# Kernel optimization log

Hardware: AMD Instinct MI355X
Metric: run time of the kernel (lower is better)

Reference implementation:

```python
import jax, jax.numpy as jnp
import numpy as np

B, S, D = 4, 2048, 1024
H, E = 8, 128  # num_head, num_dim (per-head)

def setup_inputs() -> dict:
    key = jax.random.key(0)
    ks = jax.random.split(key, 8)
    scale_in = 1.0 / np.sqrt(D)
    return {
        "q": jax.random.normal(ks[0], (B, S, D), dtype=jnp.float32),
        "k": jax.random.normal(ks[1], (B, S, D), dtype=jnp.float32),
        "v": jax.random.normal(ks[2], (B, S, D), dtype=jnp.float32),
        "Wq": jax.random.normal(ks[3], (H, D, E), dtype=jnp.float32) * scale_in,
        "Wk": jax.random.normal(ks[4], (H, D, E), dtype=jnp.float32) * scale_in,
        "Wv": jax.random.normal(ks[5], (H, D, E), dtype=jnp.float32) * scale_in,
        "Wo": jax.random.normal(ks[6], (H * E, D), dtype=jnp.float32) * (1.0 / np.sqrt(H * E)),
        "bo": jnp.zeros((D,), dtype=jnp.float32),
    }

def reference(q, k, v, Wq, Wk, Wv, Wo, bo):
    dk = jnp.asarray(E, q.dtype) ** 0.5
    # per-head projections, all heads batched: [B,H,S,E]
    qh = jnp.einsum("bsd,hde->bhse", q, Wq)
    kh = jnp.einsum("bsd,hde->bhse", k, Wk)
    vh = jnp.einsum("bsd,hde->bhse", v, Wv)
    scores = jnp.einsum("bhse,bhte->bhst", qh / dk, kh)  # [B,H,S,S]
    attn = jax.nn.softmax(scores, axis=-1)
    zh = jnp.einsum("bhst,bhte->bhse", attn, vh)  # [B,H,S,E]
    # concat heads along feature dim (head order preserved): [B,S,H*E]
    z = jnp.transpose(zh, (0, 2, 1, 3)).reshape(B, S, H * E)
    return z @ Wo + bo
```

## Files before the change

kernel.cpp:

```cpp
#include <hip/hip_runtime.h>

#define B_ 4
#define S_ 2048
#define D_ 1024
#define H_ 8
#define E_ 128

typedef __bf16 bf16_t;
typedef __bf16 bf16x8 __attribute__((ext_vector_type(8)));
typedef float f32x4 __attribute__((ext_vector_type(4)));

#define MFMA16(a, b, c) __builtin_amdgcn_mfma_f32_16x16x32_bf16(a, b, c, 0, 0, 0)

#define LDP_ 72

__device__ __forceinline__ void load_lds16(const bf16_t* g, bf16_t* l) {
    __builtin_amdgcn_global_load_lds(
        (const __attribute__((address_space(1))) unsigned int*)g,
        (__attribute__((address_space(3))) unsigned int*)l,
        16, 0, 0);
}

__device__ __forceinline__ f32x4 zero4() {
    f32x4 z = {0.f, 0.f, 0.f, 0.f};
    return z;
}

__global__ __launch_bounds__(64) void detect_dtype(const unsigned int* __restrict__ q,
                                                   int* __restrict__ flag) {
    int lane = threadIdx.x;
    int cnt = 0;
    for (int i = lane; i < 4096; i += 64) {
        unsigned e = (q[i] >> 7) & 0xFFu;
        cnt += (e >= 110u && e <= 141u) ? 1 : 0;
    }
#pragma unroll
    for (int d = 32; d; d >>= 1) cnt += __shfl_down(cnt, d);
    if (lane == 0) *flag = (cnt > 2048) ? 1 : 0;
}

__global__ __launch_bounds__(256) void convert_bf16(const void* __restrict__ in,
                                                    bf16_t* __restrict__ out,
                                                    const int* __restrict__ flagp) {
    int isb = *flagp;
    size_t i = ((size_t)blockIdx.x * 256 + threadIdx.x) * 8;
    if (isb) {
        *(bf16x8*)(out + i) = *(const bf16x8*)((const bf16_t*)in + i);
    } else {
        const float* p = (const float*)in + i;
        f32x4 lo = *(const f32x4*)p;
        f32x4 hi = *(const f32x4*)(p + 4);
        bf16x8 v;
#pragma unroll
        for (int j = 0; j < 4; j++) { v[j] = (bf16_t)lo[j]; v[4 + j] = (bf16_t)hi[j]; }
        *(bf16x8*)(out + i) = v;
    }
}

__global__ __launch_bounds__(256) void transpose_any(const void* __restrict__ in,
                                                     bf16_t* __restrict__ out,
                                                     int R, int C,
                                                     const int* __restrict__ flagp) {
    __shared__ bf16_t tile[32][33];
    int isb = *flagp;
    int bz = blockIdx.z;
    const bf16_t* inb16 = (const bf16_t*)in + (size_t)bz * R * C;
    const float*  inb32 = (const float*)in + (size_t)bz * R * C;
    bf16_t* outb = out + (size_t)bz * R * C;
    int tx = threadIdx.x & 31, ty = threadIdx.x >> 5;
    int r0 = blockIdx.y * 32, c0 = blockIdx.x * 32;
#pragma unroll
    for (int i = 0; i < 4; i++) {
        size_t idx = (size_t)(r0 + ty + i * 8) * C + c0 + tx;
        tile[ty + i * 8][tx] = isb ? inb16[idx] : (bf16_t)inb32[idx];
    }
    __syncthreads();
#pragma unroll
    for (int i = 0; i < 4; i++)
        outb[(size_t)(c0 + ty + i * 8) * R + r0 + tx] = tile[tx][ty + i * 8];
}

__global__ __launch_bounds__(256) void proj_gemm(const bf16_t* __restrict__ A,
                                                 const bf16_t* __restrict__ Wt,
                                                 bf16_t* __restrict__ Out,
                                                 int vmode, float oscale) {
    __shared__ __align__(16) bf16_t Alds[128 * 32];
    __shared__ __align__(16) bf16_t Blds[128 * 32];
    int m0 = blockIdx.x * 128;
    int h = blockIdx.y;
    const bf16_t* Bt = Wt + (size_t)h * E_ * D_;
    int t = threadIdx.x;
    int w = t >> 6, lane = t & 63;
    int quad = lane >> 4, ln = lane & 15;
    int wm = (w >> 1) * 64, wn = (w & 1) * 64;

    f32x4 acc[4][4];
#pragma unroll
    for (int i = 0; i < 4; i++)
#pragma unroll
        for (int j = 0; j < 4; j++) acc[i][j] = zero4();

    for (int k0 = 0; k0 < D_; k0 += 32) {
#pragma unroll
        for (int i = 0; i < 2; i++) {
            int base = i * 256 + w * 64;
            int G = base + lane;
            int r = G >> 2, c = (G & 3) ^ (r & 3);
            load_lds16(A + (size_t)(m0 + r) * D_ + k0 + c * 8, Alds + (size_t)base * 8);
            load_lds16(Bt + (size_t)r * D_ + k0 + c * 8, Blds + (size_t)base * 8);
        }
        asm volatile("s_waitcnt vmcnt(0)" ::: "memory");
        __syncthreads();

        bf16x8 af[4], bfr[4];
#pragma unroll
        for (int mt = 0; mt < 4; mt++) {
            int row = wm + mt * 16 + ln;
            af[mt] = *(const bf16x8*)(Alds + (size_t)row * 32 + (quad ^ (ln & 3)) * 8);
        }
#pragma unroll
        for (int nt = 0; nt < 4; nt++) {
            int row = wn + nt * 16 + ln;
            bfr[nt] = *(const bf16x8*)(Blds + (size_t)row * 32 + (quad ^ (ln & 3)) * 8);
        }
#pragma unroll
        for (int mt = 0; mt < 4; mt++)
#pragma unroll
            for (int nt = 0; nt < 4; nt++)
                acc[mt][nt] = MFMA16(af[mt], bfr[nt], acc[mt][nt]);
        __syncthreads();
    }

#pragma unroll
    for (int mt = 0; mt < 4; mt++) {
#pragma unroll
        for (int nt = 0; nt < 4; nt++) {
#pragma unroll
            for (int r = 0; r < 4; r++) {
                int grow = m0 + wm + mt * 16 + quad * 4 + r;
                int e = wn + nt * 16 + ln;
                int b = grow >> 11;
                int s = grow & 2047;
                float v = acc[mt][nt][r] * oscale;
                size_t idx;
                if (vmode == 0)
                    idx = ((size_t)((b * H_ + h) * S_ + s)) * E_ + e;
                else
                    idx = ((size_t)((b * H_ + h) * E_ + e)) * S_ + s;
                Out[idx] = (bf16_t)v;
            }
        }
    }
}

__global__ __launch_bounds__(256, 3) void flash_attn(const bf16_t* __restrict__ Qh,
                                                     const bf16_t* __restrict__ Kh,
                                                     const bf16_t* __restrict__ Vt,
                                                     bf16_t* __restrict__ Z) {
    __shared__ __align__(16) bf16_t Klds[64 * 128];
    __shared__ __align__(16) bf16_t Vlds[128 * 64];
    __shared__ __align__(16) bf16_t Plds[4 * 32 * LDP_];
    int bh = blockIdx.y;
    int qt = blockIdx.x;
    const bf16_t* Qbh = Qh + (size_t)bh * S_ * E_;
    const bf16_t* Kbh = Kh + (size_t)bh * S_ * E_;
    const bf16_t* Vbh = Vt + (size_t)bh * E_ * S_;
    int t = threadIdx.x, w = t >> 6, lane = t & 63;
    int quad = lane >> 4, ln = lane & 15;
    bf16_t* Pw = Plds + w * 32 * LDP_;

    bf16x8 qf[2][4];
#pragma unroll
    for (int mt = 0; mt < 2; mt++)
#pragma unroll
        for (int ks = 0; ks < 4; ks++)
            qf[mt][ks] = *(const bf16x8*)(Qbh + (size_t)(qt * 128 + w * 32 + mt * 16 + ln) * E_ +
                                          ks * 32 + quad * 8);

    f32x4 oacc[2][8];
#pragma unroll
    for (int mt = 0; mt < 2; mt++)
#pragma unroll
        for (int nt = 0; nt < 8; nt++) oacc[mt][nt] = zero4();
    float rsum[2][4];
#pragma unroll
    for (int mt = 0; mt < 2; mt++)
#pragma unroll
        for (int r = 0; r < 4; r++) rsum[mt][r] = 0.f;

    for (int kt = 0; kt < S_ / 64; kt++) {
#pragma unroll
        for (int j = 0; j < 4; j++) {
            int base = j * 256 + w * 64;
            int G = base + lane;
            int rK = G >> 4, cK = (G & 15) ^ (rK & 15);
            load_lds16(Kbh + (size_t)(kt * 64 + rK) * E_ + cK * 8, Klds + (size_t)base * 8);
            int rV = G >> 3, cV = (G & 7) ^ (rV & 7);
            load_lds16(Vbh + (size_t)rV * S_ + kt * 64 + cV * 8, Vlds + (size_t)base * 8);
        }
        asm volatile("s_waitcnt vmcnt(0)" ::: "memory");
        __syncthreads();

#pragma unroll
        for (int nt = 0; nt < 4; nt++) {
            f32x4 sacc[2];
            sacc[0] = zero4();
            sacc[1] = zero4();
#pragma unroll
            for (int ks = 0; ks < 4; ks++) {
                int n = nt * 16 + ln;
                bf16x8 kf = *(const bf16x8*)(Klds + (size_t)n * 128 +
                                             (((ks * 4 + quad) ^ ln) & 15) * 8);
#pragma unroll
                for (int mt = 0; mt < 2; mt++) sacc[mt] = MFMA16(qf[mt][ks], kf, sacc[mt]);
            }
#pragma unroll
            for (int mt = 0; mt < 2; mt++) {
#pragma unroll
                for (int r = 0; r < 4; r++) {
                    float p = exp2f(sacc[mt][r] - 18.0f);
                    rsum[mt][r] += p;
                    Pw[(size_t)(mt * 16 + quad * 4 + r) * LDP_ + nt * 16 + ln] = (bf16_t)p;
                }
            }
        }

        asm volatile("s_waitcnt lgkmcnt(0)" ::: "memory");

#pragma unroll
        for (int ks = 0; ks < 2; ks++) {
            bf16x8 pf[2], vf[8];
#pragma unroll
            for (int mt = 0; mt < 2; mt++)
                pf[mt] = *(const bf16x8*)(Pw + (size_t)(mt * 16 + ln) * LDP_ + ks * 32 + quad * 8);
#pragma unroll
            for (int nt = 0; nt < 8; nt++) {
                int n = nt * 16 + ln;
                vf[nt] = *(const bf16x8*)(Vlds + (size_t)n * 64 +
                                          (((ks * 4 + quad) ^ n) & 7) * 8);
            }
#pragma unroll
            for (int mt = 0; mt < 2; mt++)
#pragma unroll
                for (int nt = 0; nt < 8; nt++)
                    oacc[mt][nt] = MFMA16(pf[mt], vf[nt], oacc[mt][nt]);
        }
        __syncthreads();
    }

    float lr[2][4];
#pragma unroll
    for (int mt = 0; mt < 2; mt++)
#pragma unroll
        for (int r = 0; r < 4; r++) {
            float v = rsum[mt][r];
#pragma unroll
            for (int d = 1; d < 16; d <<= 1) v += __shfl_xor(v, d);
            lr[mt][r] = v;
        }

    int b = bh >> 3, h = bh & 7;
#pragma unroll
    for (int mt = 0; mt < 2; mt++) {
#pragma unroll
        for (int nt = 0; nt < 8; nt++) {
#pragma unroll
            for (int r = 0; r < 4; r++) {
                int s = qt * 128 + w * 32 + mt * 16 + quad * 4 + r;
                int col = h * E_ + nt * 16 + ln;
                Z[((size_t)(b * S_ + s)) * (H_ * E_) + col] =
                    (bf16_t)(oacc[mt][nt][r] / lr[mt][r]);
            }
        }
    }
}

__global__ __launch_bounds__(256) void final_gemm(const bf16_t* __restrict__ A,
                                                  const bf16_t* __restrict__ Bt,
                                                  const void* __restrict__ bias,
                                                  void* __restrict__ Out,
                                                  const int* __restrict__ flagp) {
    __shared__ __align__(16) bf16_t Alds[128 * 32];
    __shared__ __align__(16) bf16_t Blds[128 * 32];
    int isb = *flagp;
    int m0 = blockIdx.x * 128;
    int n0 = blockIdx.y * 128;
    int t = threadIdx.x;
    int w = t >> 6, lane = t & 63;
    int quad = lane >> 4, ln = lane & 15;
    int wm = (w >> 1) * 64, wn = (w & 1) * 64;

    f32x4 acc[4][4];
#pragma unroll
    for (int i = 0; i < 4; i++)
#pragma unroll
        for (int j = 0; j < 4; j++) acc[i][j] = zero4();

    for (int k0 = 0; k0 < D_; k0 += 32) {
#pragma unroll
        for (int i = 0; i < 2; i++) {
            int base = i * 256 + w * 64;
            int G = base + lane;
            int r = G >> 2, c = (G & 3) ^ (r & 3);
            load_lds16(A + (size_t)(m0 + r) * (H_ * E_) + k0 + c * 8, Alds + (size_t)base * 8);
            load_lds16(Bt + (size_t)(n0 + r) * (H_ * E_) + k0 + c * 8, Blds + (size_t)base * 8);
        }
        asm volatile("s_waitcnt vmcnt(0)" ::: "memory");
        __syncthreads();

        bf16x8 af[4], bfr[4];
#pragma unroll
        for (int mt = 0; mt < 4; mt++) {
            int row = wm + mt * 16 + ln;
            af[mt] = *(const bf16x8*)(Alds + (size_t)row * 32 + (quad ^ (ln & 3)) * 8);
        }
#pragma unroll
        for (int nt = 0; nt < 4; nt++) {
            int row = wn + nt * 16 + ln;
            bfr[nt] = *(const bf16x8*)(Blds + (size_t)row * 32 + (quad ^ (ln & 3)) * 8);
        }
#pragma unroll
        for (int mt = 0; mt < 4; mt++)
#pragma unroll
            for (int nt = 0; nt < 4; nt++)
                acc[mt][nt] = MFMA16(af[mt], bfr[nt], acc[mt][nt]);
        __syncthreads();
    }

#pragma unroll
    for (int mt = 0; mt < 4; mt++) {
#pragma unroll
        for (int nt = 0; nt < 4; nt++) {
#pragma unroll
            for (int r = 0; r < 4; r++) {
                int grow = m0 + wm + mt * 16 + quad * 4 + r;
                int col = n0 + wn + nt * 16 + ln;
                float bv = isb ? (float)((const bf16_t*)bias)[col]
                               : ((const float*)bias)[col];
                float v = acc[mt][nt][r] + bv;
                size_t idx = (size_t)grow * D_ + col;
                if (isb) ((bf16_t*)Out)[idx] = (bf16_t)v;
                else     ((float*)Out)[idx] = v;
            }
        }
    }
}

extern "C" void kernel_launch(void* const* d_in, const int* in_sizes, int n_in,
                              void* d_out, int out_size, void* d_ws, size_t ws_size,
                              hipStream_t stream) {
    const void* q  = d_in[0];
    const void* k  = d_in[1];
    const void* v  = d_in[2];
    const void* Wq = d_in[3];
    const void* Wk = d_in[4];
    const void* Wv = d_in[5];
    const void* Wo = d_in[6];
    const void* bo = d_in[7];

    int* flag = (int*)d_ws;
    bf16_t* ws = (bf16_t*)((char*)d_ws + 256);
    const size_t WSZ = (size_t)H_ * E_ * D_;
    const size_t QSZ = (size_t)B_ * H_ * S_ * E_;
    bf16_t* wqt  = ws;
    bf16_t* wkt  = wqt + WSZ;
    bf16_t* wvt  = wkt + WSZ;
    bf16_t* wot  = wvt + WSZ;
    bf16_t* conv = wot + WSZ;
    bf16_t* Qh   = conv + QSZ;
    bf16_t* Kh   = Qh + QSZ;
    bf16_t* Vt   = Kh + QSZ;
    bf16_t* Z    = conv;

    dim3 blk(256);
    detect_dtype<<<dim3(1), dim3(64), 0, stream>>>((const unsigned int*)q, flag);
    transpose_any<<<dim3(4, 32, 8), blk, 0, stream>>>(Wq, wqt, D_, E_, flag);
    transpose_any<<<dim3(4, 32, 8), blk, 0, stream>>>(Wk, wkt, D_, E_, flag);
    transpose_any<<<dim3(4, 32, 8), blk, 0, stream>>>(Wv, wvt, D_, E_, flag);
    transpose_any<<<dim3(32, 32, 1), blk, 0, stream>>>(Wo, wot, H_ * E_, D_, flag);

    const float qscale = 0.08838834764831845f * 1.44269504088896340f;

    convert_bf16<<<dim3(4096), blk, 0, stream>>>(q, conv, flag);
    proj_gemm<<<dim3(64, 8), blk, 0, stream>>>(conv, wqt, Qh, 0, qscale);
    convert_bf16<<<dim3(4096), blk, 0, stream>>>(k, conv, flag);
    proj_gemm<<<dim3(64, 8), blk, 0, stream>>>(conv, wkt, Kh, 0, 1.0f);
    convert_bf16<<<dim3(4096), blk, 0, stream>>>(v, conv, flag);
    proj_gemm<<<dim3(64, 8), blk, 0, stream>>>(conv, wvt, Vt, 1, 1.0f);

    flash_attn<<<dim3(16, 32), blk, 0, stream>>>(Qh, Kh, Vt, Z);
    final_gemm<<<dim3(64, 8), blk, 0, stream>>>(Z, wot, bo, d_out, flag);
}
```

Before: 424.5 us.

## Batch QKV projections into one launch and deepen GEMM K-tile to 64

Projection GEMMs for Q, K and V are merged into a single 3D-grid launch when the workspace is large enough, with separate bf16 conversion buffers. Both projection and output GEMMs move to a 64-wide K tile with an 8-way XOR swizzle, halving barrier count per K. The V projection swaps its MFMA operands so the transposed output is written contiguously along sequence. This uses more LDS and workspace per block, and falls back to the sequential path when workspace is small.

```diff
diff --git a/kernel.cpp b/kernel.cpp
--- a/kernel.cpp
+++ b/kernel.cpp
@@ -80,15 +80,24 @@
         outb[(size_t)(c0 + ty + i * 8) * R + r0 + tx] = tile[tx][ty + i * 8];
 }
 
-__global__ __launch_bounds__(256) void proj_gemm(const bf16_t* __restrict__ A,
-                                                 const bf16_t* __restrict__ Wt,
-                                                 bf16_t* __restrict__ Out,
-                                                 int vmode, float oscale) {
-    __shared__ __align__(16) bf16_t Alds[128 * 32];
-    __shared__ __align__(16) bf16_t Blds[128 * 32];
+__global__ __launch_bounds__(256) void proj_gemm(const bf16_t* __restrict__ Abase,
+                                                 int useZ,
+                                                 const bf16_t* __restrict__ WtBase,
+                                                 bf16_t* __restrict__ OutBase,
+                                                 float qscale, int z0) {
+    __shared__ __align__(16) bf16_t Alds[128 * 64];
+    __shared__ __align__(16) bf16_t Blds[128 * 64];
+    const size_t WSZ = (size_t)H_ * E_ * D_;
+    const size_t QSZ = (size_t)B_ * H_ * S_ * E_;
+    int z = z0 + blockIdx.z;
+    const bf16_t* A = Abase + (useZ ? (size_t)z * QSZ : 0);
+    const bf16_t* Bt = WtBase + (size_t)z * WSZ + (size_t)blockIdx.y * E_ * D_;
+    bf16_t* Out = OutBase + (size_t)z * QSZ;
+    int vmode = (z == 2);
+    float oscale = (z == 0) ? qscale : 1.0f;
+
     int m0 = blockIdx.x * 128;
     int h = blockIdx.y;
-    const bf16_t* Bt = Wt + (size_t)h * E_ * D_;
     int t = threadIdx.x;
     int w = t >> 6, lane = t & 63;
     int quad = lane >> 4, ln = lane & 15;
@@ -100,53 +109,64 @@
 #pragma unroll
         for (int j = 0; j < 4; j++) acc[i][j] = zero4();
 
-    for (int k0 = 0; k0 < D_; k0 += 32) {
-#pragma unroll
-        for (int i = 0; i < 2; i++) {
-            int base = i * 256 + w * 64;
+    for (int k0 = 0; k0 < D_; k0 += 64) {
+#pragma unroll
+        for (int j = 0; j < 4; j++) {
+            int base = j * 256 + w * 64;
             int G = base + lane;
-            int r = G >> 2, c = (G & 3) ^ (r & 3);
+            int r = G >> 3, sl = G & 7;
+            int c = sl ^ (r & 7);
             load_lds16(A + (size_t)(m0 + r) * D_ + k0 + c * 8, Alds + (size_t)base * 8);
             load_lds16(Bt + (size_t)r * D_ + k0 + c * 8, Blds + (size_t)base * 8);
         }
         asm volatile("s_waitcnt vmcnt(0)" ::: "memory");
         __syncthreads();
 
-        bf16x8 af[4], bfr[4];
-#pragma unroll
-        for (int mt = 0; mt < 4; mt++) {
-            int row = wm + mt * 16 + ln;
-            af[mt] = *(const bf16x8*)(Alds + (size_t)row * 32 + (quad ^ (ln & 3)) * 8);
-        }
+        const bf16_t* Xsrc = vmode ? Blds : Alds;
+        const bf16_t* Ysrc = vmode ? Alds : Blds;
+#pragma unroll
+        for (int ks = 0; ks < 2; ks++) {
+            bf16x8 xf[4], yf[4];
+#pragma unroll
+            for (int mt = 0; mt < 4; mt++) {
+                int row = wm + mt * 16 + ln;
+                xf[mt] = *(const bf16x8*)(Xsrc + (size_t)row * 64 +
+                                          (((ks << 2) + quad) ^ (row & 7)) * 8);
+            }
+#pragma unroll
+            for (int nt = 0; nt < 4; nt++) {
+                int row = wn + nt * 16 + ln;
+                yf[nt] = *(const bf16x8*)(Ysrc + (size_t)row * 64 +
+                                          (((ks << 2) + quad) ^ (row & 7)) * 8);
+            }
+#pragma unroll
+            for (int mt = 0; mt < 4; mt++)
+#pragma unroll
+                for (int nt = 0; nt < 4; nt++)
+                    acc[mt][nt] = MFMA16(xf[mt], yf[nt], acc[mt][nt]);
+        }
+        __syncthreads();
+    }
+
+#pragma unroll
+    for (int mt = 0; mt < 4; mt++) {
 #pragma unroll
         for (int nt = 0; nt < 4; nt++) {
-            int row = wn + nt * 16 + ln;
-            bfr[nt] = *(const bf16x8*)(Blds + (size_t)row * 32 + (quad ^ (ln & 3)) * 8);
-        }
-#pragma unroll
-        for (int mt = 0; mt < 4; mt++)
-#pragma unroll
-            for (int nt = 0; nt < 4; nt++)
-                acc[mt][nt] = MFMA16(af[mt], bfr[nt], acc[mt][nt]);
-        __syncthreads();
-    }
-
-#pragma unroll
-    for (int mt = 0; mt < 4; mt++) {
-#pragma unroll
-        for (int nt = 0; nt < 4; nt++) {
 #pragma unroll
             for (int r = 0; r < 4; r++) {
-                int grow = m0 + wm + mt * 16 + quad * 4 + r;
-                int e = wn + nt * 16 + ln;
-                int b = grow >> 11;
-                int s = grow & 2047;
+                int M = wm + mt * 16 + quad * 4 + r;
+                int N = wn + nt * 16 + ln;
                 float v = acc[mt][nt][r] * oscale;
                 size_t idx;
-                if (vmode == 0)
-                    idx = ((size_t)((b * H_ + h) * S_ + s)) * E_ + e;
-                else
-                    idx = ((size_t)((b * H_ + h) * E_ + e)) * S_ + s;
+                if (vmode == 0) {
+                    int g = m0 + M;
+                    int b = g >> 11, s = g & 2047;
+                    idx = ((size_t)((b * H_ + h) * S_ + s)) * E_ + N;
+                } else {
+                    int g = m0 + N;
+                    int b = g >> 11, s = g & 2047;
+                    idx = ((size_t)((b * H_ + h) * E_ + M)) * S_ + s;
+                }
                 Out[idx] = (bf16_t)v;
             }
         }
@@ -280,8 +300,8 @@
                                                   const void* __restrict__ bias,
                                                   void* __restrict__ Out,
                                                   const int* __restrict__ flagp) {
-    __shared__ __align__(16) bf16_t Alds[128 * 32];
-    __shared__ __align__(16) bf16_t Blds[128 * 32];
+    __shared__ __align__(16) bf16_t Alds[128 * 64];
+    __shared__ __align__(16) bf16_t Blds[128 * 64];
     int isb = *flagp;
     int m0 = blockIdx.x * 128;
     int n0 = blockIdx.y * 128;
@@ -296,34 +316,40 @@
 #pragma unroll
         for (int j = 0; j < 4; j++) acc[i][j] = zero4();
 
-    for (int k0 = 0; k0 < D_; k0 += 32) {
-#pragma unroll
-        for (int i = 0; i < 2; i++) {
-            int base = i * 256 + w * 64;
+    for (int k0 = 0; k0 < D_; k0 += 64) {
+#pragma unroll
+        for (int j = 0; j < 4; j++) {
+            int base = j * 256 + w * 64;
             int G = base + lane;
-            int r = G >> 2, c = (G & 3) ^ (r & 3);
+            int r = G >> 3, sl = G & 7;
+            int c = sl ^ (r & 7);
             load_lds16(A + (size_t)(m0 + r) * (H_ * E_) + k0 + c * 8, Alds + (size_t)base * 8);
             load_lds16(Bt + (size_t)(n0 + r) * (H_ * E_) + k0 + c * 8, Blds + (size_t)base * 8);
         }
         asm volatile("s_waitcnt vmcnt(0)" ::: "memory");
         __syncthreads();
 
-        bf16x8 af[4], bfr[4];
-#pragma unroll
-        for (int mt = 0; mt < 4; mt++) {
-            int row = wm + mt * 16 + ln;
-            af[mt] = *(const bf16x8*)(Alds + (size_t)row * 32 + (quad ^ (ln & 3)) * 8);
-        }
-#pragma unroll
-        for (int nt = 0; nt < 4; nt++) {
-            int row = wn + nt * 16 + ln;
-            bfr[nt] = *(const bf16x8*)(Blds + (size_t)row * 32 + (quad ^ (ln & 3)) * 8);
-        }
-#pragma unroll
-        for (int mt = 0; mt < 4; mt++)
-#pragma unroll
-            for (int nt = 0; nt < 4; nt++)
-                acc[mt][nt] = MFMA16(af[mt], bfr[nt], acc[mt][nt]);
+#pragma unroll
+        for (int ks = 0; ks < 2; ks++) {
+            bf16x8 af[4], bfr[4];
+#pragma unroll
+            for (int mt = 0; mt < 4; mt++) {
+                int row = wm + mt * 16 + ln;
+                af[mt] = *(const bf16x8*)(Alds + (size_t)row * 64 +
+                                          (((ks << 2) + quad) ^ (row & 7)) * 8);
+            }
+#pragma unroll
+            for (int nt = 0; nt < 4; nt++) {
+                int row = wn + nt * 16 + ln;
+                bfr[nt] = *(const bf16x8*)(Blds + (size_t)row * 64 +
+                                           (((ks << 2) + quad) ^ (row & 7)) * 8);
+            }
+#pragma unroll
+            for (int mt = 0; mt < 4; mt++)
+#pragma unroll
+                for (int nt = 0; nt < 4; nt++)
+                    acc[mt][nt] = MFMA16(af[mt], bfr[nt], acc[mt][nt]);
+        }
         __syncthreads();
     }
 
@@ -359,35 +385,55 @@
     const void* bo = d_in[7];
 
     int* flag = (int*)d_ws;
-    bf16_t* ws = (bf16_t*)((char*)d_ws + 256);
+    bf16_t* arena = (bf16_t*)((char*)d_ws + 256);
     const size_t WSZ = (size_t)H_ * E_ * D_;
     const size_t QSZ = (size_t)B_ * H_ * S_ * E_;
-    bf16_t* wqt  = ws;
-    bf16_t* wkt  = wqt + WSZ;
-    bf16_t* wvt  = wkt + WSZ;
-    bf16_t* wot  = wvt + WSZ;
-    bf16_t* conv = wot + WSZ;
-    bf16_t* Qh   = conv + QSZ;
-    bf16_t* Kh   = Qh + QSZ;
-    bf16_t* Vt   = Kh + QSZ;
-    bf16_t* Z    = conv;
+    bf16_t* wqt = arena;
+    bf16_t* wkt = wqt + WSZ;
+    bf16_t* wvt = wkt + WSZ;
+    bf16_t* wot = wvt + WSZ;
+
+    const size_t bigBytes = 256 + 2 * (4 * WSZ + 6 * QSZ);
+    const bool big = (ws_size >= bigBytes);
 
     dim3 blk(256);
+    const float qscale = 0.08838834764831845f * 1.44269504088896340f;
+
     detect_dtype<<<dim3(1), dim3(64), 0, stream>>>((const unsigned int*)q, flag);
     transpose_any<<<dim3(4, 32, 8), blk, 0, stream>>>(Wq, wqt, D_, E_, flag);
     transpose_any<<<dim3(4, 32, 8), blk, 0, stream>>>(Wk, wkt, D_, E_, flag);
     transpose_any<<<dim3(4, 32, 8), blk, 0, stream>>>(Wv, wvt, D_, E_, flag);
     transpose_any<<<dim3(32, 32, 1), blk, 0, stream>>>(Wo, wot, H_ * E_, D_, flag);
 
-    const float qscale = 0.08838834764831845f * 1.44269504088896340f;
-
-    convert_bf16<<<dim3(4096), blk, 0, stream>>>(q, conv, flag);
-    proj_gemm<<<dim3(64, 8), blk, 0, stream>>>(conv, wqt, Qh, 0, qscale);
-    convert_bf16<<<dim3(4096), blk, 0, stream>>>(k, conv, flag);
-    proj_gemm<<<dim3(64, 8), blk, 0, stream>>>(conv, wkt, Kh, 0, 1.0f);
-    convert_bf16<<<dim3(4096), blk, 0, stream>>>(v, conv, flag);
-    proj_gemm<<<dim3(64, 8), blk, 0, stream>>>(conv, wvt, Vt, 1, 1.0f);
-
-    flash_attn<<<dim3(16, 32), blk, 0, stream>>>(Qh, Kh, Vt, Z);
-    final_gemm<<<dim3(64, 8), blk, 0, stream>>>(Z, wot, bo, d_out, flag);
-}
+    if (big) {
+        bf16_t* conv0 = wot + WSZ;
+        bf16_t* conv1 = conv0 + QSZ;
+        bf16_t* conv2 = conv1 + QSZ;
+        bf16_t* Qh = conv2 + QSZ;
+        bf16_t* Kh = Qh + QSZ;
+        bf16_t* Vt = Kh + QSZ;
+        bf16_t* Z  = conv0;
+
+        convert_bf16<<<dim3(4096), blk, 0, stream>>>(q, conv0, flag);
+        convert_bf16<<<dim3(4096), blk, 0, stream>>>(k, conv1, flag);
+        convert_bf16<<<dim3(4096), blk, 0, stream>>>(v, conv2, flag);
+        proj_gemm<<<dim3(64, 8, 3), blk, 0, stream>>>(conv0, 1, wqt, Qh, qscale, 0);
+        flash_attn<<<dim3(16, 32), blk, 0, stream>>>(Qh, Kh, Vt, Z);
+        final_gemm<<<dim3(64, 8), blk, 0, stream>>>(Z, wot, bo, d_out, flag);
+    } else {
+        bf16_t* conv = wot + WSZ;
+        bf16_t* Qh = conv + QSZ;
+        bf16_t* Kh = Qh + QSZ;
+        bf16_t* Vt = Kh + QSZ;
+        bf16_t* Z  = conv;
+
+        convert_bf16<<<dim3(4096), blk, 0, stream>>>(q, conv, flag);
+        proj_gemm<<<dim3(64, 8, 1), blk, 0, stream>>>(conv, 0, wqt, Qh, qscale, 0);
+        convert_bf16<<<dim3(4096), blk, 0, stream>>>(k, conv, flag);
+        proj_gemm<<<dim3(64, 8, 1), blk, 0, stream>>>(conv, 0, wqt, Qh, qscale, 1);
+        convert_bf16<<<dim3(4096), blk, 0, stream>>>(v, conv, flag);
+        proj_gemm<<<dim3(64, 8, 1), blk, 0, stream>>>(conv, 0, wqt, Qh, qscale, 2);
+        flash_attn<<<dim3(16, 32), blk, 0, stream>>>(Qh, Kh, Vt, Z);
+        final_gemm<<<dim3(64, 8), blk, 0, stream>>>(Z, wot, bo, d_out, flag);
+    }
+}
```

New measurement: 406.9 us. 4.1% less time.
